# Kernel tuning notes

Hardware: AMD Instinct MI355X
Metric: run time of the kernel (lower is better)

The kernel has to match this reference:

```python
import jax, jax.numpy as jnp
import numpy as np

B, L, DIN, DOUT, H, N, NLAYERS, NRES, NSPECIES = 32, 2048, 5, 5, 256, 32, 4, 3, 100


def conv1d(x, w, b, pad):
    # x: (B, Cin, L), w: (Cout, Cin, K)
    y = jax.lax.conv_general_dilated(x, w, (1,), [(pad, pad)], dimension_numbers=('NCH', 'OIH', 'NCH'))
    return y + b[None, :, None]


def layer_norm_c(x, g, b):
    # LayerNorm over channel dim of (B, H, L) (matches norm(x.transpose(-1,-2)).transpose(-1,-2))
    mu = x.mean(1, keepdims=True)
    v = ((x - mu) ** 2).mean(1, keepdims=True)
    return (x - mu) / jnp.sqrt(v + 1e-5) * g[None, :, None] + b[None, :, None]


def dss_layer(x, log_dt, lam_re, lam_im, W_re, W_im, D, glu_w, glu_b):
    # Bidirectional diagonal state-space (DSS) layer, transposed layout (B, H, L).
    Bb, Hh, Ll = x.shape
    dt = jnp.exp(log_dt)                                  # (H,)
    lam = lam_re + 1j * lam_im                            # (N,) with Re(lam) < 0
    pos = jnp.arange(Ll)
    # Vandermonde: E[h,n,l] = exp(dt[h] * lam[n] * l)
    E = jnp.exp(dt[:, None, None] * lam[None, :, None] * pos[None, None, :])  # (H,N,L) complex
    W = W_re + 1j * W_im                                  # (2,H,N) fwd/bwd kernels
    k = jnp.einsum('chn,hnl->chl', W, E).real             # (2,H,L)
    zpad = jnp.zeros_like(k[0])
    k2 = jnp.concatenate([k[0], zpad], -1) + jnp.concatenate([zpad, k[1][:, ::-1]], -1)  # (H,2L)
    # FFT circular conv of length 2L -> linear conv, keep first L
    y = jnp.fft.irfft(jnp.fft.rfft(x, 2 * Ll) * jnp.fft.rfft(k2, 2 * Ll)[None], 2 * Ll)[..., :Ll]
    y = y + D[None, :, None] * x
    y = jax.nn.gelu(y, approximate=False)
    # postact GLU via position-wise linear H -> 2H
    z = jnp.einsum('oh,bhl->bol', glu_w, y) + glu_b[None, :, None]
    return z[:, :Hh] * jax.nn.sigmoid(z[:, Hh:])


def setup_inputs():
    key = jax.random.key(0)
    ks = jax.random.split(key, 20)
    g = lambda i, shape, s=0.05: jax.random.normal(ks[i], shape, jnp.float32) * s
    inp = {}
    inp['x'] = jax.random.normal(ks[0], (B, DIN, L), jnp.float32)
    inp['xs'] = jax.random.randint(ks[1], (B,), 0, NSPECIES)
    inp['enc_w'] = g(2, (H, DIN, 15))
    inp['enc_b'] = jnp.zeros((H,), jnp.float32)
    inp['res_w1'] = g(3, (NRES, H, H, 3), 0.02)
    inp['res_b1'] = jnp.zeros((NRES, H), jnp.float32)
    inp['res_w2'] = g(4, (NRES, H, H, 3), 0.02)
    inp['res_b2'] = jnp.zeros((NRES, H), jnp.float32)
    inp['log_dt'] = jax.random.uniform(ks[5], (NLAYERS, H), jnp.float32, float(np.log(1e-3)), float(np.log(1e-1)))
    inp['lam_re'] = -(0.1 + jax.random.uniform(ks[6], (NLAYERS, N), jnp.float32))
    inp['lam_im'] = jnp.broadcast_to(jnp.pi * jnp.arange(N, dtype=jnp.float32), (NLAYERS, N)) + 0.0
    inp['W_re'] = g(7, (NLAYERS, 2, H, N), 0.1)
    inp['W_im'] = g(8, (NLAYERS, 2, H, N), 0.1)
    inp['D'] = g(9, (NLAYERS, H), 1.0)
    inp['glu_w'] = g(10, (NLAYERS, 2 * H, H))
    inp['glu_b'] = jnp.zeros((NLAYERS, 2 * H), jnp.float32)
    inp['ln_g'] = jnp.ones((NLAYERS, H), jnp.float32)
    inp['ln_b'] = jnp.zeros((NLAYERS, H), jnp.float32)
    inp['dec_w'] = g(11, (DOUT, H, 15))
    inp['dec_b'] = jnp.zeros((DOUT,), jnp.float32)
    inp['sp_emb'] = g(12, (NSPECIES, H), 0.02)
    inp['h1_w'] = g(13, (128, 256)); inp['h1_b'] = jnp.zeros((128,), jnp.float32)
    inp['h2_w'] = g(14, (64, 128)); inp['h2_b'] = jnp.zeros((64,), jnp.float32)
    inp['h3_w'] = g(15, (32, 64)); inp['h3_b'] = jnp.zeros((32,), jnp.float32)
    inp['h4_w'] = g(16, (1, 32)); inp['h4_b'] = jnp.zeros((1,), jnp.float32)
    return inp


def _forward(x, xs, enc_w, enc_b, res_w1, res_b1, res_w2, res_b2, log_dt, lam_re, lam_im, W_re, W_im, D, glu_w, glu_b, ln_g, ln_b, dec_w, dec_b, sp_emb, h1_w, h1_b, h2_w, h2_b, h3_w, h3_b, h4_w, h4_b):
    h = conv1d(x, enc_w, enc_b, 7)
    for i in range(NRES):  # L1Block resnet stack (dropout/BN are identity at eval)
        r = jax.nn.relu(conv1d(h, res_w1[i], res_b1[i], 1))
        r = conv1d(r, res_w2[i], res_b2[i], 1)
        h = jax.nn.relu(r + h)
    for i in range(NLAYERS):  # post-norm DSS blocks
        z = dss_layer(h, log_dt[i], lam_re[i], lam_im[i], W_re[i], W_im[i], D[i], glu_w[i], glu_b[i])
        h = layer_norm_c(z + h, ln_g[i], ln_b[i])
    h = h + sp_emb[xs][:, :, None]  # species encoder (embed_before=False)
    seq_emb = h
    agg = h.mean(-1)  # (B, H)
    r = jax.nn.elu(agg @ h1_w.T + h1_b)
    r = jax.nn.elu(r @ h2_w.T + h2_b)
    r = jax.nn.elu(r @ h3_w.T + h3_b)
    reg_y = r @ h4_w.T + h4_b
    dec = conv1d(h, dec_w, dec_b, 7)
    return dec, seq_emb, reg_y


def reference(x, xs, enc_w, enc_b, res_w1, res_b1, res_w2, res_b2, log_dt, lam_re, lam_im, W_re, W_im, D, glu_w, glu_b, ln_g, ln_b, dec_w, dec_b, sp_emb, h1_w, h1_b, h2_w, h2_b, h3_w, h3_b, h4_w, h4_b):
    return _forward(x, xs, enc_w, enc_b, res_w1, res_b1, res_w2, res_b2, log_dt, lam_re, lam_im, W_re, W_im, D, glu_w, glu_b, ln_g, ln_b, dec_w, dec_b, sp_emb, h1_w, h1_b, h2_w, h2_b, h3_w, h3_b, h4_w, h4_b)
```

## Files before the change

kernel.cpp:

```cpp
#include <hip/hip_runtime.h>
#include <math.h>

#define B 32
#define L 2048
#define DIN 5
#define DOUT 5
#define H 256
#define NST 32
#define NLAYERS 4
#define NRES 3
#define CHUNK 128
#define NCH 16
#define LSEQ (B*H*L)

typedef __attribute__((ext_vector_type(8))) _Float16 half8;
typedef __attribute__((ext_vector_type(4))) float f32x4;

__device__ __forceinline__ float gelu_exact(float v) {
    return 0.5f * v * (1.0f + erff(v * 0.7071067811865475f));
}
#define SWZ(r) ((((r) ^ ((r) >> 2)) & 3))
#define LDIDX(l, c) ((l)*281 + ((c)>>5)*35 + ((c)&31))

__global__ void k_wenc(const float* __restrict__ ew, _Float16* __restrict__ wenc) {
    int idx = blockIdx.x*256 + threadIdx.x;
    if (idx >= 256*96) return;
    int o = idx / 96, kk = idx % 96;
    int ci = kk >> 4, k = kk & 15;
    float v = (ci < DIN && k < 15) ? ew[(o*DIN + ci)*15 + k] : 0.f;
    wenc[idx] = (_Float16)v;
}

__global__ __launch_bounds__(256) void k_enc(const float* __restrict__ x,
        const _Float16* __restrict__ wenc, const float* __restrict__ bias,
        _Float16* __restrict__ out) {
    __shared__ _Float16 a_lds[3*128*32];
    __shared__ _Float16 b_lds[3*128*32];
    const int tid = threadIdx.x;
    const int mbase = blockIdx.x * 128;
    const int oh = blockIdx.y;
    const int b = mbase >> 11;
    const int lbase = mbase & 2047;
    const int lane = tid & 63;
    const int w = tid >> 6;
    const int wm = (w >> 1) * 64, wn = (w & 1) * 64;
    const int fr = lane & 15, kg = lane >> 4;

    #pragma unroll
    for (int i = 0; i < 6; ++i) {
        int g = i*256 + tid;
        int r = g / 12, rem = g % 12;
        int ks = rem >> 2, q = rem & 3;
        int kk0 = ks*32 + q*8;
        int ci = kk0 >> 4, k0 = kk0 & 15;
        half8 va;
        #pragma unroll
        for (int e = 0; e < 8; ++e) {
            int k = k0 + e;
            int l = lbase + r - 7 + k;
            float v = (ci < DIN && k < 15 && l >= 0 && l < L)
                        ? x[((size_t)(b*DIN + ci))*L + l] : 0.f;
            va[e] = (_Float16)v;
        }
        *(half8*)&a_lds[ks*4096 + r*32 + ((q ^ SWZ(r))*8)] = va;
        uint4 vb = *(const uint4*)&wenc[(size_t)(oh*128 + r)*96 + kk0];
        *(uint4*)&b_lds[ks*4096 + r*32 + ((q ^ SWZ(r))*8)] = vb;
    }
    __syncthreads();
    f32x4 acc[4][4];
    #pragma unroll
    for (int i = 0; i < 4; ++i)
        #pragma unroll
        for (int j = 0; j < 4; ++j)
            #pragma unroll
            for (int k = 0; k < 4; ++k) acc[i][j][k] = 0.f;
    #pragma unroll
    for (int ks = 0; ks < 3; ++ks) {
        half8 af[4], bfr[4];
        #pragma unroll
        for (int mf = 0; mf < 4; ++mf) {
            int ra = wm + mf*16 + fr;
            af[mf] = *(const half8*)&a_lds[ks*4096 + ra*32 + ((kg ^ SWZ(ra))*8)];
        }
        #pragma unroll
        for (int nf = 0; nf < 4; ++nf) {
            int rb = wn + nf*16 + fr;
            bfr[nf] = *(const half8*)&b_lds[ks*4096 + rb*32 + ((kg ^ SWZ(rb))*8)];
        }
        #pragma unroll
        for (int mf = 0; mf < 4; ++mf)
            #pragma unroll
            for (int nf = 0; nf < 4; ++nf)
                acc[mf][nf] = __builtin_amdgcn_mfma_f32_16x16x32_f16(af[mf], bfr[nf], acc[mf][nf], 0, 0, 0);
    }
    #pragma unroll
    for (int nf = 0; nf < 4; ++nf) {
        int o = oh*128 + wn + nf*16 + fr;
        float bo = bias[o];
        #pragma unroll
        for (int mf = 0; mf < 4; ++mf)
            #pragma unroll
            for (int rg = 0; rg < 4; ++rg) {
                size_t m = (size_t)mbase + wm + mf*16 + kg*4 + rg;
                out[m*256 + o] = (_Float16)(acc[mf][nf][rg] + bo);
            }
    }
}

__global__ void k_wpack(const float* __restrict__ w1, const float* __restrict__ w2,
                        _Float16* __restrict__ wpk) {
    int idx = blockIdx.x*256 + threadIdx.x;
    if (idx >= NRES*2*3*65536) return;
    int ci = idx & 255;
    int o  = (idx >> 8) & 255;
    int k  = (idx >> 16) % 3;
    int cv = idx / (3*65536);
    const float* src = (cv & 1) ? w2 : w1;
    wpk[idx] = (_Float16)src[(((cv>>1)*H + o)*H + ci)*3 + k];
}

__global__ __launch_bounds__(256) void k_t_cf16(const _Float16* __restrict__ in,
        _Float16* __restrict__ out) {
    __shared__ float t[64][65];
    int tid = threadIdx.x;
    int l0 = blockIdx.x*64, c0 = blockIdx.y*64, b = blockIdx.z;
    #pragma unroll
    for (int i = 0; i < 16; ++i) {
        int idx = i*256 + tid;
        int l = idx >> 6, c = idx & 63;
        t[c][l] = (float)in[((size_t)b*L + l0 + l)*256 + c0 + c];
    }
    __syncthreads();
    #pragma unroll
    for (int i = 0; i < 16; ++i) {
        int idx = i*256 + tid;
        int c = idx >> 6, l = idx & 63;
        out[((size_t)(b*H + c0 + c))*L + l0 + l] = (_Float16)t[c][l];
    }
}

__global__ __launch_bounds__(256) void k_t16(const _Float16* __restrict__ in,
                                             _Float16* __restrict__ out) {
    __shared__ float t[64][65];
    int tid = threadIdx.x;
    int l0 = blockIdx.x*64, c0 = blockIdx.y*64, b = blockIdx.z;
    #pragma unroll
    for (int i = 0; i < 16; ++i) {
        int idx = i*256 + tid;
        int c = idx >> 6, l = idx & 63;
        t[c][l] = (float)in[((size_t)(b*H + c0 + c))*L + l0 + l];
    }
    __syncthreads();
    #pragma unroll
    for (int i = 0; i < 16; ++i) {
        int idx = i*256 + tid;
        int l = idx >> 6, c = idx & 63;
        out[((size_t)b*L + l0 + l)*256 + c0 + c] = (_Float16)t[c][l];
    }
}

template<bool RESID>
__global__ __launch_bounds__(256, 2) void k_cv3(const _Float16* __restrict__ xin,
        const _Float16* __restrict__ wpk, const float* __restrict__ bias,
        const _Float16* __restrict__ resid, _Float16* __restrict__ out) {
    __shared__ _Float16 a_lds[128*32];
    __shared__ _Float16 b_lds[256*32];
    __shared__ float    ep[32*256];
    const int tid = threadIdx.x;
    const int mbase = blockIdx.x * 128;
    const int lane = tid & 63;
    const int w = tid >> 6;
    const int wm = (w >> 1) * 64, wo = (w & 1) * 128;
    const int fr = lane & 15, kg = lane >> 4;

    const int r0s = tid >> 2, q0 = tid & 3;
    const int sq = SWZ(r0s);
    const int awA0 = r0s*32 + ((q0 ^ sq) * 8);
    const int awA1 = (64 + r0s)*32 + ((q0 ^ SWZ(64 + r0s)) * 8);

    f32x4 acc[4][8];
    #pragma unroll
    for (int i = 0; i < 4; ++i)
        #pragma unroll
        for (int j = 0; j < 8; ++j)
            #pragma unroll
            for (int k = 0; k < 4; ++k) acc[i][j][k] = 0.f;

    uint4 pa0, pa1, pb[4];
    auto loadstep = [&](int kk, uint4& a0, uint4& a1, uint4 (&bb)[4]) {
        const int koff = kk >> 3, cic = kk & 7;
        const int cb = cic*32 + q0*8;
        {
            int m = mbase + r0s;
            int ll = (m & (L-1)) + koff - 1;
            a0 = (ll >= 0 && ll < L) ? *(const uint4*)&xin[((size_t)(m + koff - 1))*256 + cb]
                                     : make_uint4(0,0,0,0);
            int m1 = mbase + 64 + r0s;
            int l1 = (m1 & (L-1)) + koff - 1;
            a1 = (l1 >= 0 && l1 < L) ? *(const uint4*)&xin[((size_t)(m1 + koff - 1))*256 + cb]
                                     : make_uint4(0,0,0,0);
        }
        #pragma unroll
        for (int u = 0; u < 4; ++u)
            bb[u] = *(const uint4*)&wpk[((size_t)(koff*256 + u*64 + r0s))*256 + cb];
    };
    loadstep(0, pa0, pa1, pb);
    for (int kk = 0; kk < 24; ++kk) {
        __syncthreads();
        *(uint4*)&a_lds[awA0] = pa0;
        *(uint4*)&a_lds[awA1] = pa1;
        #pragma unroll
        for (int u = 0; u < 4; ++u)
            *(uint4*)&b_lds[(u*64 + r0s)*32 + ((q0 ^ sq)*8)] = pb[u];
        uint4 na0 = make_uint4(0,0,0,0), na1 = na0, nb[4] = {na0, na0, na0, na0};
        if (kk < 23) loadstep(kk+1, na0, na1, nb);
        __syncthreads();
        half8 af[4];
        #pragma unroll
        for (int mf = 0; mf < 4; ++mf) {
            int ra = wm + mf*16 + fr;
            af[mf] = *(const half8*)&a_lds[ra*32 + ((kg ^ SWZ(ra)) * 8)];
        }
        #pragma unroll
        for (int nf = 0; nf < 8; ++nf) {
            int rb = wo + nf*16 + fr;
            half8 bfr = *(const half8*)&b_lds[rb*32 + ((kg ^ SWZ(rb)) * 8)];
            #pragma unroll
            for (int mf = 0; mf < 4; ++mf)
                acc[mf][nf] = __builtin_amdgcn_mfma_f32_16x16x32_f16(af[mf], bfr, acc[mf][nf], 0, 0, 0);
        }
        pa0 = na0; pa1 = na1;
        #pragma unroll
        for (int u = 0; u < 4; ++u) pb[u] = nb[u];
    }
    float bo8[8];
    #pragma unroll
    for (int nf = 0; nf < 8; ++nf) bo8[nf] = bias[wo + nf*16 + fr];
    const int er = tid >> 3, eoc = (tid & 7) * 32;
    #pragma unroll
    for (int mf = 0; mf < 4; ++mf) {
        __syncthreads();
        #pragma unroll
        for (int nf = 0; nf < 8; ++nf) {
            int o = wo + nf*16 + fr;
            int srb = (w >> 1)*16 + kg*4;
            #pragma unroll
            for (int rg = 0; rg < 4; ++rg)
                ep[(srb + rg)*256 + o] = acc[mf][nf][rg] + bo8[nf];
        }
        __syncthreads();
        size_t m = (size_t)mbase + mf*16 + (er < 16 ? er : 48 + er);
        #pragma unroll
        for (int u = 0; u < 4; ++u) {
            float4 v0 = *(float4*)&ep[er*256 + eoc + u*8];
            float4 v1 = *(float4*)&ep[er*256 + eoc + u*8 + 4];
            float vv[8] = {v0.x, v0.y, v0.z, v0.w, v1.x, v1.y, v1.z, v1.w};
            if (RESID) {
                half8 rv = *(const half8*)&resid[m*256 + eoc + u*8];
                #pragma unroll
                for (int e = 0; e < 8; ++e) vv[e] += (float)rv[e];
            }
            half8 hv;
            #pragma unroll
            for (int e = 0; e < 8; ++e) hv[e] = (_Float16)fmaxf(vv[e], 0.f);
            *(half8*)&out[m*256 + eoc + u*8] = hv;
        }
    }
}

__global__ __launch_bounds__(128) void k_wzp(const float* __restrict__ log_dt,
        const float* __restrict__ lam_re, const float* __restrict__ lam_im,
        _Float16* __restrict__ zp, float4* __restrict__ zwbuf, int layer) {
    int hh = blockIdx.x;
    int t = threadIdx.x;
    int dn = t >> 1, c = t & 1, dir = dn >> 5, n = dn & 31;
    float dt = expf(log_dt[layer*H + hh]);
    float a  = dt * lam_re[layer*NST + n];
    float bi = dt * lam_im[layer*NST + n];
    float er = expf(a);
    float zre = er * cosf(bi), zim = er * sinf(bi);
    if (c == 0 && dir == 0) {
        float eC = expf(a * (float)CHUNK);
        float s, co; sincosf(bi * (float)CHUNK, &s, &co);
        zwbuf[hh*NST + n] = make_float4(zre, zim, eC*co, eC*s);
    }
    _Float16* dst = &zp[(size_t)hh*16384 + t*128];
    float cr = 1.f, ci = 0.f;
    for (int p = 0; p < 128; ++p) {
        float val = c ? ci : cr;
        dst[dir ? p : (127 - p)] = (_Float16)val;
        float nr = cr*zre - ci*zim;
        float ni = cr*zim + ci*zre;
        cr = nr; ci = ni;
    }
}

__global__ __launch_bounds__(128) void k_wkern(const float* __restrict__ log_dt,
        const float* __restrict__ lam_re, const float* __restrict__ lam_im,
        const float* __restrict__ W_re, const float* __restrict__ W_im,
        const float* __restrict__ Dv, const float* __restrict__ gw,
        _Float16* __restrict__ wbig, _Float16* __restrict__ wg, int layer) {
    __shared__ float kf[128], kb[128];
    __shared__ float E[128*129];
    const int hh = blockIdx.x;
    const int t = threadIdx.x;
    float dt = expf(log_dt[layer*H + hh]);
    float skf = 0.f, skb = 0.f;
    for (int n = 0; n < 32; ++n) {
        float a  = dt * lam_re[layer*NST + n];
        float bi = dt * lam_im[layer*NST + n];
        float wfr = W_re[((layer*2+0)*H + hh)*NST + n];
        float wfi = W_im[((layer*2+0)*H + hh)*NST + n];
        float wbr = W_re[((layer*2+1)*H + hh)*NST + n];
        float wbi = W_im[((layer*2+1)*H + hh)*NST + n];
        float e0 = expf(a*t), s0, c0; sincosf(bi*t, &s0, &c0);
        float zr0 = e0*c0, zi0 = e0*s0;
        skf = fmaf(wfr, zr0, skf) - wfi*zi0;
        skb = fmaf(wbr, zr0, skb) - wbi*zi0;
        float e1 = expf(a*(t+1)), s1, c1; sincosf(bi*(t+1), &s1, &c1);
        float zr1 = e1*c1, zi1 = e1*s1;
        E[t*129 + n]      = wfr*zr1 - wfi*zi1;
        E[t*129 + 32 + n] = -(wfr*zi1 + wfi*zr1);
        float e2 = expf(a*(127-t)), s2, c2; sincosf(bi*(127-t), &s2, &c2);
        float zr2 = e2*c2, zi2 = e2*s2;
        E[t*129 + 64 + n] = wbr*zr2 - wbi*zi2;
        E[t*129 + 96 + n] = -(wbr*zi2 + wbi*zr2);
    }
    kf[t] = skf + ((t == 0) ? Dv[layer*H + hh] : 0.f);
    kb[t] = skb;
    __syncthreads();
    _Float16* dst = &wbig[(size_t)hh*32768];
    for (int idx = t; idx < 128*256; idx += 128) {
        int tt = idx >> 8, k = idx & 255;
        float v;
        if (k < 128) v = (k <= tt) ? kf[tt - k] : kb[k - tt - 1];
        else         v = E[tt*129 + (k - 128)];
        dst[idx] = (_Float16)v;
    }
    const float* gsrc = &gw[(size_t)layer*131072 + (size_t)hh*512];
    _Float16* gdst = &wg[(size_t)hh*512];
    for (int j = t; j < 512; j += 128) gdst[j] = (_Float16)gsrc[j];
}

__global__ void k_wdec(const float* __restrict__ dw, _Float16* __restrict__ wdk) {
    int idx = blockIdx.x*256 + threadIdx.x;
    if (idx >= 15*16*256) return;
    int cfull = idx & 255;
    int o = (idx >> 8) & 15;
    int k = idx >> 12;
    float v = (o < DOUT) ? dw[(o*H + cfull)*15 + k] : 0.f;
    int cc = cfull >> 5, cl = cfull & 31;
    int cq = cl >> 3, cb = cl & 7;
    wdk[cc*7680 + (k*16 + o)*32 + ((cq ^ SWZ(o))*8) + cb] = (_Float16)v;
}

__global__ __launch_bounds__(256) void k_dss(const _Float16* __restrict__ hm16,
        const _Float16* __restrict__ zp, const _Float16* __restrict__ wbig,
        const float4* __restrict__ zwb, _Float16* __restrict__ y16, int layer) {
    __shared__ _Float16 xbuf[4*64*32];
    __shared__ _Float16 bbuf[2*128*32];
    __shared__ float    sbuf[64*128];
    _Float16* sb16 = (_Float16*)sbuf;

    const int tid = threadIdx.x;
    const int hh = blockIdx.x;
    const int b0 = blockIdx.y * 4;
    const int lane = tid & 63;
    const int w = tid >> 6;
    const int wn = w * 32;
    const int fr = lane & 15, kg = lane >> 4;

    #pragma unroll
    for (int i = 0; i < 4; ++i) {
        int g = i*256 + tid;
        int m = g >> 4, gi = g & 15;
        int kc = gi >> 2, q = gi & 3;
        uint4 v = *(const uint4*)&hm16[((size_t)((b0 + (m>>4))*H + hh))*L
                                       + (m&15)*128 + kc*32 + q*8];
        *(uint4*)&xbuf[kc*2048 + m*32 + ((q ^ SWZ(m))*8)] = v;
    }

    f32x4 acc1[4][2];
    #pragma unroll
    for (int i = 0; i < 4; ++i)
        #pragma unroll
        for (int j = 0; j < 2; ++j)
            #pragma unroll
            for (int k = 0; k < 4; ++k) acc1[i][j][k] = 0.f;
    const _Float16* zb = &zp[(size_t)hh*16384];
    const int gr0 = tid >> 2, gq0 = tid & 3;
    const int gr1 = 64 + gr0;
    uint4 pb0 = *(const uint4*)&zb[gr0*128 + gq0*8];
    uint4 pb1 = *(const uint4*)&zb[gr1*128 + gq0*8];
    for (int kc = 0; kc < 4; ++kc) {
        __syncthreads();
        *(uint4*)&bbuf[(kc&1)*4096 + gr0*32 + ((gq0 ^ SWZ(gr0))*8)] = pb0;
        *(uint4*)&bbuf[(kc&1)*4096 + gr1*32 + ((gq0 ^ SWZ(gr1))*8)] = pb1;
        if (kc < 3) {
            pb0 = *(const uint4*)&zb[gr0*128 + (kc+1)*32 + gq0*8];
            pb1 = *(const uint4*)&zb[gr1*128 + (kc+1)*32 + gq0*8];
        }
        __syncthreads();
        half8 af[4], bf2[2];
        #pragma unroll
        for (int mf = 0; mf < 4; ++mf) {
            int ra = mf*16 + fr;
            af[mf] = *(const half8*)&xbuf[kc*2048 + ra*32 + ((kg ^ SWZ(ra))*8)];
        }
        #pragma unroll
        for (int nf = 0; nf < 2; ++nf) {
            int rb = wn + nf*16 + fr;
            bf2[nf] = *(const half8*)&bbuf[(kc&1)*4096 + rb*32 + ((kg ^ SWZ(rb))*8)];
        }
        #pragma unroll
        for (int mf = 0; mf < 4; ++mf)
            #pragma unroll
            for (int nf = 0; nf < 2; ++nf)
                acc1[mf][nf] = __builtin_amdgcn_mfma_f32_16x16x32_f16(af[mf], bf2[nf], acc1[mf][nf], 0, 0, 0);
    }
    #pragma unroll
    for (int mf = 0; mf < 4; ++mf)
        #pragma unroll
        for (int nf = 0; nf < 2; ++nf)
            #pragma unroll
            for (int rg = 0; rg < 4; ++rg)
                sbuf[(mf*16 + kg*4 + rg)*128 + wn + nf*16 + fr] = acc1[mf][nf][rg];
    __syncthreads();

    {
        int b_loc = tid >> 6, dn = tid & 63;
        int dir = dn >> 5, n = dn & 31;
        float4 z4 = zwb[hh*NST + n];
        float zcre = z4.z, zcim = z4.w;
        int q1 = n >> 3, e1 = n & 7;
        float pre = 0.f, pim = 0.f;
        for (int s = 0; s < NCH; ++s) {
            int ch = dir ? (NCH - 1 - s) : s;
            int m = b_loc*16 + ch;
            bbuf[(dir*2 + 0)*2048 + m*32 + ((q1 ^ SWZ(m))*8) + e1] = (_Float16)pre;
            bbuf[(dir*2 + 1)*2048 + m*32 + ((q1 ^ SWZ(m))*8) + e1] = (_Float16)pim;
            float cre = sbuf[m*128 + dn*2];
            float cim = sbuf[m*128 + dn*2 + 1];
            float nre = fmaf(zcre, pre, fmaf(-zcim, pim, cre));
            float nim = fmaf(zcre, pim, fmaf(zcim, pre, cim));
            pre = nre; pim = nim;
        }
    }
    __syncthreads();

    f32x4 acc3[4][2];
    #pragma unroll
    for (int i = 0; i < 4; ++i)
        #pragma unroll
        for (int j = 0; j < 2; ++j)
            #pragma unroll
            for (int k = 0; k < 4; ++k) acc3[i][j][k] = 0.f;
    const _Float16* wb = &wbig[(size_t)hh*32768];
    pb0 = *(const uint4*)&wb[gr0*256 + gq0*8];
    pb1 = *(const uint4*)&wb[gr1*256 + gq0*8];
    for (int kc = 0; kc < 8; ++kc) {
        __syncthreads();
        *(uint4*)&sb16[(kc&1)*4096 + gr0*32 + ((gq0 ^ SWZ(gr0))*8)] = pb0;
        *(uint4*)&sb16[(kc&1)*4096 + gr1*32 + ((gq0 ^ SWZ(gr1))*8)] = pb1;
        if (kc < 7) {
            pb0 = *(const uint4*)&wb[gr0*256 + (kc+1)*32 + gq0*8];
            pb1 = *(const uint4*)&wb[gr1*256 + (kc+1)*32 + gq0*8];
        }
        __syncthreads();
        half8 af[4], bf2[2];
        #pragma unroll
        for (int mf = 0; mf < 4; ++mf) {
            int ra = mf*16 + fr;
            af[mf] = (kc < 4)
                ? *(const half8*)&xbuf[kc*2048 + ra*32 + ((kg ^ SWZ(ra))*8)]
                : *(const half8*)&bbuf[(kc-4)*2048 + ra*32 + ((kg ^ SWZ(ra))*8)];
        }
        #pragma unroll
        for (int nf = 0; nf < 2; ++nf) {
            int rb = wn + nf*16 + fr;
            bf2[nf] = *(const half8*)&sb16[(kc&1)*4096 + rb*32 + ((kg ^ SWZ(rb))*8)];
        }
        #pragma unroll
        for (int mf = 0; mf < 4; ++mf)
            #pragma unroll
            for (int nf = 0; nf < 2; ++nf)
                acc3[mf][nf] = __builtin_amdgcn_mfma_f32_16x16x32_f16(af[mf], bf2[nf], acc3[mf][nf], 0, 0, 0);
    }
    __syncthreads();
    _Float16* yst = sb16;
    #pragma unroll
    for (int mf = 0; mf < 4; ++mf) {
        #pragma unroll
        for (int rg = 0; rg < 4; ++rg) {
            int m = mf*16 + kg*4 + rg;
            #pragma unroll
            for (int nf = 0; nf < 2; ++nf) {
                int t = wn + nf*16 + fr;
                yst[m*136 + t] = (_Float16)gelu_exact(acc3[mf][nf][rg]);
            }
        }
    }
    __syncthreads();
    {
        int r = tid >> 2, tc = (tid & 3) * 32;
        size_t gb = ((size_t)((b0 + (r>>4))*H + hh))*L + (r&15)*128;
        #pragma unroll
        for (int u = 0; u < 4; ++u)
            *(half8*)&y16[gb + tc + u*8] = *(half8*)&yst[r*136 + tc + u*8];
    }
}

__global__ __launch_bounds__(256) void k_glu16(const _Float16* __restrict__ yt,
        const _Float16* __restrict__ wg, const float* __restrict__ bias,
        _Float16* __restrict__ zc) {
    __shared__ _Float16 a_lds[128*32];
    __shared__ _Float16 b_lds[128*32];
    __shared__ float    ep[32*64];
    const int tid = threadIdx.x;
    const int mbase = blockIdx.x * 128;
    const int o0 = blockIdx.y * 64;
    const int lane = tid & 63;
    const int w = tid >> 6;
    const int wm = (w >> 1) * 64, wn = (w & 1) * 32;
    const int fr = lane & 15, kg = lane >> 4;
    const int r0s = tid >> 2, q0 = tid & 3;
    const int r1s = 64 + r0s;
    const int aw0 = r0s*32 + ((q0 ^ SWZ(r0s)) * 8);
    const int aw1 = r1s*32 + ((q0 ^ SWZ(r1s)) * 8);
    const int og0 = o0 + r0s;
    const int og1 = 256 + o0 + r0s;

    f32x4 accg[4][2], accs[4][2];
    #pragma unroll
    for (int i = 0; i < 4; ++i)
        #pragma unroll
        for (int j = 0; j < 2; ++j)
            #pragma unroll
            for (int k = 0; k < 4; ++k) { accg[i][j][k] = 0.f; accs[i][j][k] = 0.f; }

    uint4 pa0, pa1, pb0, pb1;
    auto loadstep = [&](int kc, uint4& a0, uint4& a1, uint4& b0, uint4& b1) {
        const int cb = kc*32 + q0*8;
        a0 = *(const uint4*)&yt[((size_t)(mbase + r0s))*256 + cb];
        a1 = *(const uint4*)&yt[((size_t)(mbase + r1s))*256 + cb];
        b0 = *(const uint4*)&wg[((size_t)og0)*256 + cb];
        b1 = *(const uint4*)&wg[((size_t)og1)*256 + cb];
    };
    loadstep(0, pa0, pa1, pb0, pb1);
    for (int kc = 0; kc < 8; ++kc) {
        __syncthreads();
        *(uint4*)&a_lds[aw0] = pa0;
        *(uint4*)&a_lds[aw1] = pa1;
        *(uint4*)&b_lds[aw0] = pb0;
        *(uint4*)&b_lds[aw1] = pb1;
        uint4 na0 = make_uint4(0,0,0,0), na1 = na0, nb0 = na0, nb1 = na0;
        if (kc < 7) loadstep(kc+1, na0, na1, nb0, nb1);
        __syncthreads();
        half8 af[4], bg[2], bs[2];
        #pragma unroll
        for (int mf = 0; mf < 4; ++mf) {
            int ra = wm + mf*16 + fr;
            af[mf] = *(const half8*)&a_lds[ra*32 + ((kg ^ SWZ(ra)) * 8)];
        }
        #pragma unroll
        for (int nf = 0; nf < 2; ++nf) {
            int rb = wn + nf*16 + fr;
            bg[nf] = *(const half8*)&b_lds[rb*32 + ((kg ^ SWZ(rb)) * 8)];
            int rb2 = 64 + rb;
            bs[nf] = *(const half8*)&b_lds[rb2*32 + ((kg ^ SWZ(rb2)) * 8)];
        }
        #pragma unroll
        for (int mf = 0; mf < 4; ++mf)
            #pragma unroll
            for (int nf = 0; nf < 2; ++nf) {
                accg[mf][nf] = __builtin_amdgcn_mfma_f32_16x16x32_f16(af[mf], bg[nf], accg[mf][nf], 0, 0, 0);
                accs[mf][nf] = __builtin_amdgcn_mfma_f32_16x16x32_f16(af[mf], bs[nf], accs[mf][nf], 0, 0, 0);
            }
        pa0 = na0; pa1 = na1; pb0 = nb0; pb1 = nb1;
    }
    float b0v[2], b1v[2];
    #pragma unroll
    for (int nf = 0; nf < 2; ++nf) {
        int o = o0 + wn + nf*16 + fr;
        b0v[nf] = bias[o]; b1v[nf] = bias[256 + o];
    }
    const int er = tid >> 3, eoc = (tid & 7) * 8;
    #pragma unroll
    for (int mf = 0; mf < 4; ++mf) {
        __syncthreads();
        #pragma unroll
        for (int nf = 0; nf < 2; ++nf) {
            int ol = wn + nf*16 + fr;
            int srb = (w >> 1)*16 + kg*4;
            #pragma unroll
            for (int rg = 0; rg < 4; ++rg) {
                float g = accg[mf][nf][rg] + b0v[nf];
                float s = accs[mf][nf][rg] + b1v[nf];
                ep[(srb + rg)*64 + ol] = g / (1.f + expf(-s));
            }
        }
        __syncthreads();
        size_t m = (size_t)mbase + mf*16 + (er < 16 ? er : 48 + er);
        float4 v0 = *(float4*)&ep[er*64 + eoc];
        float4 v1 = *(float4*)&ep[er*64 + eoc + 4];
        half8 hv;
        hv[0]=(_Float16)v0.x; hv[1]=(_Float16)v0.y; hv[2]=(_Float16)v0.z; hv[3]=(_Float16)v0.w;
        hv[4]=(_Float16)v1.x; hv[5]=(_Float16)v1.y; hv[6]=(_Float16)v1.z; hv[7]=(_Float16)v1.w;
        *(half8*)&zc[m*256 + o0 + eoc] = hv;
    }
}

template<bool SP>
__global__ __launch_bounds__(256) void k_ln2(const _Float16* __restrict__ zc,
        _Float16* __restrict__ hm, const float* __restrict__ g, const float* __restrict__ bb,
        const int* __restrict__ xs, const float* __restrict__ emb,
        float* __restrict__ outseq) {
    __shared__ float tl[8992];
    int tid = threadIdx.x;
    int b = blockIdx.y;
    int l0 = blockIdx.x * 32;
    for (int j = tid; j < 1024; j += 256) {
        int c = j >> 2, l8 = (j & 3) * 8;
        half8 v = *(const half8*)&hm[((size_t)(b*H + c))*L + l0 + l8];
        #pragma unroll
        for (int e = 0; e < 8; ++e) tl[LDIDX(l8 + e, c)] = (float)v[e];
    }
    __syncthreads();
    int r = tid >> 3, p = tid & 7;
    float v[32];
    float sum = 0.f, ss = 0.f;
    const _Float16* zrow = &zc[((size_t)(b*L + l0 + r))*256 + p*32];
    #pragma unroll
    for (int q = 0; q < 4; ++q) {
        half8 z8 = *(const half8*)&zrow[q*8];
        #pragma unroll
        for (int i = 0; i < 8; ++i) {
            float hv = tl[LDIDX(r, p*32 + q*8 + i)];
            float vv = (float)z8[i] + hv;
            v[q*8+i] = vv;
            sum += vv; ss = fmaf(vv, vv, ss);
        }
    }
    sum += __shfl_xor(sum, 1); ss += __shfl_xor(ss, 1);
    sum += __shfl_xor(sum, 2); ss += __shfl_xor(ss, 2);
    sum += __shfl_xor(sum, 4); ss += __shfl_xor(ss, 4);
    float mu = sum * (1.f/256.f);
    float var = ss * (1.f/256.f) - mu*mu;
    float rs = rsqrtf(var + 1e-5f);
    int sp = SP ? xs[b] : 0;
    #pragma unroll
    for (int q = 0; q < 32; ++q) {
        int c = p*32 + q;
        float val = (v[q] - mu) * rs * g[c] + bb[c];
        if (SP) val += emb[sp*H + c];
        tl[LDIDX(r, c)] = val;
    }
    __syncthreads();
    for (int j = tid; j < 1024; j += 256) {
        int c = j >> 2, l8 = (j & 3) * 8;
        float fv[8];
        half8 hv;
        #pragma unroll
        for (int e = 0; e < 8; ++e) {
            fv[e] = tl[LDIDX(l8 + e, c)];
            hv[e] = (_Float16)fv[e];
        }
        *(half8*)&hm[((size_t)(b*H + c))*L + l0 + l8] = hv;
        if (SP) {
            *(float4*)&outseq[((size_t)(b*H + c))*L + l0 + l8] = make_float4(fv[0],fv[1],fv[2],fv[3]);
            *(float4*)&outseq[((size_t)(b*H + c))*L + l0 + l8 + 4] = make_float4(fv[4],fv[5],fv[6],fv[7]);
        }
    }
}

__global__ __launch_bounds__(128) void k_dec(const _Float16* __restrict__ ht,
        const _Float16* __restrict__ wdk, const float* __restrict__ bias,
        float* __restrict__ outdec) {
    __shared__ _Float16 a_lds[160*32];
    __shared__ _Float16 b_lds[15*16*32];
    const int tid = threadIdx.x;
    const int mbase = blockIdx.x * 128;
    const int b = mbase >> 11;
    const int lbase = mbase & 2047;
    const int lane = tid & 63;
    const int w = tid >> 6;
    const int fr = lane & 15, kg = lane >> 4;
    const int rs = tid >> 2, q0 = tid & 3;
    f32x4 acc[4];
    #pragma unroll
    for (int i = 0; i < 4; ++i)
        #pragma unroll
        for (int k = 0; k < 4; ++k) acc[i][k] = 0.f;
    for (int cc = 0; cc < 8; ++cc) {
        __syncthreads();
        #pragma unroll
        for (int ps = 0; ps < 5; ++ps) {
            int r = ps*32 + rs;
            if (r < 142) {
                int l = lbase - 7 + r;
                uint4 v = (l >= 0 && l < L) ? *(const uint4*)&ht[((size_t)(b*L + l))*256 + cc*32 + q0*8]
                                            : make_uint4(0,0,0,0);
                *(uint4*)&a_lds[r*32 + ((q0 ^ SWZ(r))*8)] = v;
            }
        }
        for (int jj = tid; jj < 960; jj += 128)
            *(uint4*)&b_lds[jj*8] = *(const uint4*)&wdk[cc*7680 + jj*8];
        __syncthreads();
        #pragma unroll
        for (int k = 0; k < 15; ++k) {
            half8 bfr = *(const half8*)&b_lds[(k*16 + fr)*32 + ((kg ^ SWZ(fr))*8)];
            #pragma unroll
            for (int mf = 0; mf < 4; ++mf) {
                int ra = w*64 + mf*16 + fr + k;
                half8 af = *(const half8*)&a_lds[ra*32 + ((kg ^ SWZ(ra))*8)];
                acc[mf] = __builtin_amdgcn_mfma_f32_16x16x32_f16(af, bfr, acc[mf], 0, 0, 0);
            }
        }
    }
    if (fr < DOUT) {
        float bo = bias[fr];
        #pragma unroll
        for (int mf = 0; mf < 4; ++mf)
            #pragma unroll
            for (int rg = 0; rg < 4; ++rg) {
                int m = mbase + w*64 + mf*16 + kg*4 + rg;
                outdec[((size_t)(b*DOUT + fr))*L + (m & 2047)] = acc[mf][rg] + bo;
            }
    }
}

__global__ __launch_bounds__(256) void k_agg(const _Float16* __restrict__ h, float* __restrict__ agg) {
    __shared__ float red[256];
    int bc = blockIdx.x;
    int tid = threadIdx.x;
    half8 v = *(const half8*)&h[(size_t)bc*L + tid*8];
    float s = 0.f;
    #pragma unroll
    for (int e = 0; e < 8; ++e) s += (float)v[e];
    red[tid] = s; __syncthreads();
    for (int k = 128; k > 0; k >>= 1) {
        if (tid < k) red[tid] += red[tid+k];
        __syncthreads();
    }
    if (tid == 0) agg[bc] = red[0] * (1.f/(float)L);
}

__global__ __launch_bounds__(128) void k_mlp(const float* __restrict__ agg,
        const float* __restrict__ w1, const float* __restrict__ b1,
        const float* __restrict__ w2, const float* __restrict__ b2,
        const float* __restrict__ w3, const float* __restrict__ b3,
        const float* __restrict__ w4, const float* __restrict__ b4,
        float* __restrict__ outreg) {
    __shared__ float a0[256], r1[128], r2[64], r3[32];
    int b = blockIdx.x, tid = threadIdx.x;
    a0[tid] = agg[b*256 + tid];
    a0[tid+128] = agg[b*256 + tid + 128];
    __syncthreads();
    {
        float s = b1[tid];
        for (int k = 0; k < 256; ++k) s = fmaf(w1[tid*256+k], a0[k], s);
        r1[tid] = s > 0.f ? s : expm1f(s);
    }
    __syncthreads();
    if (tid < 64) {
        float s = b2[tid];
        for (int k = 0; k < 128; ++k) s = fmaf(w2[tid*128+k], r1[k], s);
        r2[tid] = s > 0.f ? s : expm1f(s);
    }
    __syncthreads();
    if (tid < 32) {
        float s = b3[tid];
        for (int k = 0; k < 64; ++k) s = fmaf(w3[tid*64+k], r2[k], s);
        r3[tid] = s > 0.f ? s : expm1f(s);
    }
    __syncthreads();
    if (tid == 0) {
        float s = b4[0];
        for (int k = 0; k < 32; ++k) s = fmaf(w4[k], r3[k], s);
        outreg[b] = s;
    }
}

extern "C" void kernel_launch(void* const* d_in, const int* in_sizes, int n_in,
                              void* d_out, int out_size, void* d_ws, size_t ws_size,
                              hipStream_t stream) {
    const float* x      = (const float*)d_in[0];
    const int*   xs     = (const int*)d_in[1];
    const float* enc_w  = (const float*)d_in[2];
    const float* enc_b  = (const float*)d_in[3];
    const float* res_w1 = (const float*)d_in[4];
    const float* res_b1 = (const float*)d_in[5];
    const float* res_w2 = (const float*)d_in[6];
    const float* res_b2 = (const float*)d_in[7];
    const float* log_dt = (const float*)d_in[8];
    const float* lam_re = (const float*)d_in[9];
    const float* lam_im = (const float*)d_in[10];
    const float* W_re   = (const float*)d_in[11];
    const float* W_im   = (const float*)d_in[12];
    const float* Dv     = (const float*)d_in[13];
    const float* glu_w  = (const float*)d_in[14];
    const float* glu_b  = (const float*)d_in[15];
    const float* ln_g   = (const float*)d_in[16];
    const float* ln_b   = (const float*)d_in[17];
    const float* dec_w  = (const float*)d_in[18];
    const float* dec_b  = (const float*)d_in[19];
    const float* sp_emb = (const float*)d_in[20];
    const float* h1_w = (const float*)d_in[21]; const float* h1_b = (const float*)d_in[22];
    const float* h2_w = (const float*)d_in[23]; const float* h2_b = (const float*)d_in[24];
    const float* h3_w = (const float*)d_in[25]; const float* h3_b = (const float*)d_in[26];
    const float* h4_w = (const float*)d_in[27]; const float* h4_b = (const float*)d_in[28];

    float* ws   = (float*)d_ws;
    _Float16* hm16 = (_Float16*)ws;
    float* t1   = ws + (size_t)LSEQ;
    float* t2   = ws + (size_t)2*LSEQ;
    _Float16* xb  = (_Float16*)t1;
    _Float16* xa  = (_Float16*)t1 + (size_t)LSEQ;
    _Float16* wpk = (_Float16*)t2;
    _Float16* yt   = (_Float16*)t1;
    _Float16* wbig = (_Float16*)t1 + (size_t)LSEQ;
    _Float16* zp   = wbig + (size_t)H*32768;
    _Float16* y16  = (_Float16*)t2;
    _Float16* zc16 = (_Float16*)t2;
    _Float16* dect = (_Float16*)t1;
    float* tail = ws + (size_t)3*LSEQ;
    _Float16* wg  = (_Float16*)tail;
    float4* zwb = (float4*)(tail + 65536);
    float* aggb = tail + 65536 + 32768;
    _Float16* wdk = (_Float16*)(aggb + 8192);
    _Float16* wenc = wdk + 61440;

    float* outdec = (float*)d_out;
    float* outseq = outdec + B*DOUT*L;
    float* outreg = outseq + (size_t)LSEQ;

    k_wenc<<<96, 256, 0, stream>>>(enc_w, wenc);
    k_enc<<<dim3(B*L/128, 2), 256, 0, stream>>>(x, wenc, enc_b, xa);

    k_wpack<<<(NRES*2*3*65536 + 255)/256, 256, 0, stream>>>(res_w1, res_w2, wpk);
    for (int r = 0; r < NRES; ++r) {
        k_cv3<false><<<B*L/128, 256, 0, stream>>>(
            xa, wpk + (size_t)(r*2+0)*3*65536, res_b1 + r*H, nullptr, xb);
        k_cv3<true><<<B*L/128, 256, 0, stream>>>(
            xb, wpk + (size_t)(r*2+1)*3*65536, res_b2 + r*H, xa, xa);
    }
    k_t_cf16<<<dim3(L/64, H/64, B), 256, 0, stream>>>(xa, hm16);

    for (int i = 0; i < NLAYERS; ++i) {
        k_wzp<<<H, 128, 0, stream>>>(log_dt, lam_re, lam_im, zp, zwb, i);
        k_wkern<<<H, 128, 0, stream>>>(log_dt, lam_re, lam_im, W_re, W_im, Dv, glu_w,
                                       wbig, wg, i);
        k_dss<<<dim3(H, 8), 256, 0, stream>>>(hm16, zp, wbig, zwb, y16, i);
        k_t16<<<dim3(L/64, H/64, B), 256, 0, stream>>>(y16, yt);
        k_glu16<<<dim3(B*L/128, 4), 256, 0, stream>>>(yt, wg, glu_b + i*512, zc16);
        if (i < NLAYERS - 1)
            k_ln2<false><<<dim3(L/32, B), 256, 0, stream>>>(zc16, hm16, ln_g + i*H, ln_b + i*H,
                                                            nullptr, nullptr, nullptr);
        else
            k_ln2<true><<<dim3(L/32, B), 256, 0, stream>>>(zc16, hm16, ln_g + i*H, ln_b + i*H,
                                                           xs, sp_emb, outseq);
    }

    k_agg<<<B*H, 256, 0, stream>>>(hm16, aggb);
    k_mlp<<<B, 128, 0, stream>>>(aggb, h1_w, h1_b, h2_w, h2_b, h3_w, h3_b, h4_w, h4_b, outreg);
    k_t16<<<dim3(L/64, H/64, B), 256, 0, stream>>>(hm16, dect);
    k_wdec<<<(15*16*256 + 255)/256, 256, 0, stream>>>(dec_w, wdk);
    k_dec<<<B*L/128, 128, 0, stream>>>(dect, wdk, dec_b, outdec);
}
```

Before: 1.126 ms.

## Halve batch tile in DSS kernel and restructure double-buffered pipeline with one barrier

The DSS chunked-scan kernel now processes 2 batches per block instead of 4, which doubles the grid and shrinks LDS and accumulator use so more blocks fit per CU (launch_bounds 256,4). The double-buffered weight staging loops are restructured to prefetch one stage ahead with a single barrier per iteration instead of two. Half the threads now sit idle during the serial scan phase. Weight tiles are reloaded twice as often in aggregate.

```diff
diff --git a/kernel.cpp b/kernel.cpp
--- a/kernel.cpp
+++ b/kernel.cpp
@@ -354,35 +354,35 @@
     wdk[cc*7680 + (k*16 + o)*32 + ((cq ^ SWZ(o))*8) + cb] = (_Float16)v;
 }
 
-__global__ __launch_bounds__(256) void k_dss(const _Float16* __restrict__ hm16,
+__global__ __launch_bounds__(256, 4) void k_dss(const _Float16* __restrict__ hm16,
         const _Float16* __restrict__ zp, const _Float16* __restrict__ wbig,
         const float4* __restrict__ zwb, _Float16* __restrict__ y16, int layer) {
-    __shared__ _Float16 xbuf[4*64*32];
+    __shared__ _Float16 xbuf[4*32*32];
     __shared__ _Float16 bbuf[2*128*32];
-    __shared__ float    sbuf[64*128];
+    __shared__ float    sbuf[32*128];
     _Float16* sb16 = (_Float16*)sbuf;
 
     const int tid = threadIdx.x;
     const int hh = blockIdx.x;
-    const int b0 = blockIdx.y * 4;
+    const int b0 = blockIdx.y * 2;
     const int lane = tid & 63;
     const int w = tid >> 6;
     const int wn = w * 32;
     const int fr = lane & 15, kg = lane >> 4;
 
     #pragma unroll
-    for (int i = 0; i < 4; ++i) {
+    for (int i = 0; i < 2; ++i) {
         int g = i*256 + tid;
         int m = g >> 4, gi = g & 15;
         int kc = gi >> 2, q = gi & 3;
         uint4 v = *(const uint4*)&hm16[((size_t)((b0 + (m>>4))*H + hh))*L
                                        + (m&15)*128 + kc*32 + q*8];
-        *(uint4*)&xbuf[kc*2048 + m*32 + ((q ^ SWZ(m))*8)] = v;
-    }
-
-    f32x4 acc1[4][2];
-    #pragma unroll
-    for (int i = 0; i < 4; ++i)
+        *(uint4*)&xbuf[kc*1024 + m*32 + ((q ^ SWZ(m))*8)] = v;
+    }
+
+    f32x4 acc1[2][2];
+    #pragma unroll
+    for (int i = 0; i < 2; ++i)
         #pragma unroll
         for (int j = 0; j < 2; ++j)
             #pragma unroll
@@ -390,22 +390,29 @@
     const _Float16* zb = &zp[(size_t)hh*16384];
     const int gr0 = tid >> 2, gq0 = tid & 3;
     const int gr1 = 64 + gr0;
+    const int bw0 = gr0*32 + ((gq0 ^ SWZ(gr0))*8);
+    const int bw1 = gr1*32 + ((gq0 ^ SWZ(gr1))*8);
     uint4 pb0 = *(const uint4*)&zb[gr0*128 + gq0*8];
     uint4 pb1 = *(const uint4*)&zb[gr1*128 + gq0*8];
+    *(uint4*)&bbuf[bw0] = pb0;
+    *(uint4*)&bbuf[bw1] = pb1;
+    pb0 = *(const uint4*)&zb[gr0*128 + 32 + gq0*8];
+    pb1 = *(const uint4*)&zb[gr1*128 + 32 + gq0*8];
+    __syncthreads();
     for (int kc = 0; kc < 4; ++kc) {
-        __syncthreads();
-        *(uint4*)&bbuf[(kc&1)*4096 + gr0*32 + ((gq0 ^ SWZ(gr0))*8)] = pb0;
-        *(uint4*)&bbuf[(kc&1)*4096 + gr1*32 + ((gq0 ^ SWZ(gr1))*8)] = pb1;
         if (kc < 3) {
-            pb0 = *(const uint4*)&zb[gr0*128 + (kc+1)*32 + gq0*8];
-            pb1 = *(const uint4*)&zb[gr1*128 + (kc+1)*32 + gq0*8];
-        }
-        __syncthreads();
-        half8 af[4], bf2[2];
-        #pragma unroll
-        for (int mf = 0; mf < 4; ++mf) {
+            *(uint4*)&bbuf[((kc+1)&1)*4096 + bw0] = pb0;
+            *(uint4*)&bbuf[((kc+1)&1)*4096 + bw1] = pb1;
+            if (kc < 2) {
+                pb0 = *(const uint4*)&zb[gr0*128 + (kc+2)*32 + gq0*8];
+                pb1 = *(const uint4*)&zb[gr1*128 + (kc+2)*32 + gq0*8];
+            }
+        }
+        half8 af[2], bf2[2];
+        #pragma unroll
+        for (int mf = 0; mf < 2; ++mf) {
             int ra = mf*16 + fr;
-            af[mf] = *(const half8*)&xbuf[kc*2048 + ra*32 + ((kg ^ SWZ(ra))*8)];
+            af[mf] = *(const half8*)&xbuf[kc*1024 + ra*32 + ((kg ^ SWZ(ra))*8)];
         }
         #pragma unroll
         for (int nf = 0; nf < 2; ++nf) {
@@ -413,13 +420,14 @@
             bf2[nf] = *(const half8*)&bbuf[(kc&1)*4096 + rb*32 + ((kg ^ SWZ(rb))*8)];
         }
         #pragma unroll
-        for (int mf = 0; mf < 4; ++mf)
+        for (int mf = 0; mf < 2; ++mf)
             #pragma unroll
             for (int nf = 0; nf < 2; ++nf)
                 acc1[mf][nf] = __builtin_amdgcn_mfma_f32_16x16x32_f16(af[mf], bf2[nf], acc1[mf][nf], 0, 0, 0);
-    }
-    #pragma unroll
-    for (int mf = 0; mf < 4; ++mf)
+        __syncthreads();
+    }
+    #pragma unroll
+    for (int mf = 0; mf < 2; ++mf)
         #pragma unroll
         for (int nf = 0; nf < 2; ++nf)
             #pragma unroll
@@ -429,28 +437,30 @@
 
     {
         int b_loc = tid >> 6, dn = tid & 63;
-        int dir = dn >> 5, n = dn & 31;
-        float4 z4 = zwb[hh*NST + n];
-        float zcre = z4.z, zcim = z4.w;
-        int q1 = n >> 3, e1 = n & 7;
-        float pre = 0.f, pim = 0.f;
-        for (int s = 0; s < NCH; ++s) {
-            int ch = dir ? (NCH - 1 - s) : s;
-            int m = b_loc*16 + ch;
-            bbuf[(dir*2 + 0)*2048 + m*32 + ((q1 ^ SWZ(m))*8) + e1] = (_Float16)pre;
-            bbuf[(dir*2 + 1)*2048 + m*32 + ((q1 ^ SWZ(m))*8) + e1] = (_Float16)pim;
-            float cre = sbuf[m*128 + dn*2];
-            float cim = sbuf[m*128 + dn*2 + 1];
-            float nre = fmaf(zcre, pre, fmaf(-zcim, pim, cre));
-            float nim = fmaf(zcre, pim, fmaf(zcim, pre, cim));
-            pre = nre; pim = nim;
-        }
-    }
-    __syncthreads();
-
-    f32x4 acc3[4][2];
-    #pragma unroll
-    for (int i = 0; i < 4; ++i)
+        if (b_loc < 2) {
+            int dir = dn >> 5, n = dn & 31;
+            float4 z4 = zwb[hh*NST + n];
+            float zcre = z4.z, zcim = z4.w;
+            int q1 = n >> 3, e1 = n & 7;
+            float pre = 0.f, pim = 0.f;
+            for (int s = 0; s < NCH; ++s) {
+                int ch = dir ? (NCH - 1 - s) : s;
+                int m = b_loc*16 + ch;
+                bbuf[(dir*2 + 0)*1024 + m*32 + ((q1 ^ SWZ(m))*8) + e1] = (_Float16)pre;
+                bbuf[(dir*2 + 1)*1024 + m*32 + ((q1 ^ SWZ(m))*8) + e1] = (_Float16)pim;
+                float cre = sbuf[m*128 + dn*2];
+                float cim = sbuf[m*128 + dn*2 + 1];
+                float nre = fmaf(zcre, pre, fmaf(-zcim, pim, cre));
+                float nim = fmaf(zcre, pim, fmaf(zcim, pre, cim));
+                pre = nre; pim = nim;
+            }
+        }
+    }
+    __syncthreads();
+
+    f32x4 acc3[2][2];
+    #pragma unroll
+    for (int i = 0; i < 2; ++i)
         #pragma unroll
         for (int j = 0; j < 2; ++j)
             #pragma unroll
@@ -458,22 +468,27 @@
     const _Float16* wb = &wbig[(size_t)hh*32768];
     pb0 = *(const uint4*)&wb[gr0*256 + gq0*8];
     pb1 = *(const uint4*)&wb[gr1*256 + gq0*8];
+    *(uint4*)&sb16[bw0] = pb0;
+    *(uint4*)&sb16[bw1] = pb1;
+    pb0 = *(const uint4*)&wb[gr0*256 + 32 + gq0*8];
+    pb1 = *(const uint4*)&wb[gr1*256 + 32 + gq0*8];
+    __syncthreads();
     for (int kc = 0; kc < 8; ++kc) {
-        __syncthreads();
-        *(uint4*)&sb16[(kc&1)*4096 + gr0*32 + ((gq0 ^ SWZ(gr0))*8)] = pb0;
-        *(uint4*)&sb16[(kc&1)*4096 + gr1*32 + ((gq0 ^ SWZ(gr1))*8)] = pb1;
         if (kc < 7) {
-            pb0 = *(const uint4*)&wb[gr0*256 + (kc+1)*32 + gq0*8];
-            pb1 = *(const uint4*)&wb[gr1*256 + (kc+1)*32 + gq0*8];
-        }
-        __syncthreads();
-        half8 af[4], bf2[2];
-        #pragma unroll
-        for (int mf = 0; mf < 4; ++mf) {
+            *(uint4*)&sb16[((kc+1)&1)*4096 + bw0] = pb0;
+            *(uint4*)&sb16[((kc+1)&1)*4096 + bw1] = pb1;
+            if (kc < 6) {
+                pb0 = *(const uint4*)&wb[gr0*256 + (kc+2)*32 + gq0*8];
+                pb1 = *(const uint4*)&wb[gr1*256 + (kc+2)*32 + gq0*8];
+            }
+        }
+        half8 af[2], bf2[2];
+        #pragma unroll
+        for (int mf = 0; mf < 2; ++mf) {
             int ra = mf*16 + fr;
             af[mf] = (kc < 4)
-                ? *(const half8*)&xbuf[kc*2048 + ra*32 + ((kg ^ SWZ(ra))*8)]
-                : *(const half8*)&bbuf[(kc-4)*2048 + ra*32 + ((kg ^ SWZ(ra))*8)];
+                ? *(const half8*)&xbuf[kc*1024 + ra*32 + ((kg ^ SWZ(ra))*8)]
+                : *(const half8*)&bbuf[(kc-4)*1024 + ra*32 + ((kg ^ SWZ(ra))*8)];
         }
         #pragma unroll
         for (int nf = 0; nf < 2; ++nf) {
@@ -481,15 +496,15 @@
             bf2[nf] = *(const half8*)&sb16[(kc&1)*4096 + rb*32 + ((kg ^ SWZ(rb))*8)];
         }
         #pragma unroll
-        for (int mf = 0; mf < 4; ++mf)
+        for (int mf = 0; mf < 2; ++mf)
             #pragma unroll
             for (int nf = 0; nf < 2; ++nf)
                 acc3[mf][nf] = __builtin_amdgcn_mfma_f32_16x16x32_f16(af[mf], bf2[nf], acc3[mf][nf], 0, 0, 0);
-    }
-    __syncthreads();
+        __syncthreads();
+    }
     _Float16* yst = sb16;
     #pragma unroll
-    for (int mf = 0; mf < 4; ++mf) {
+    for (int mf = 0; mf < 2; ++mf) {
         #pragma unroll
         for (int rg = 0; rg < 4; ++rg) {
             int m = mf*16 + kg*4 + rg;
@@ -502,11 +517,10 @@
     }
     __syncthreads();
     {
-        int r = tid >> 2, tc = (tid & 3) * 32;
+        int r = tid >> 3, tc = (tid & 7) * 16;
         size_t gb = ((size_t)((b0 + (r>>4))*H + hh))*L + (r&15)*128;
-        #pragma unroll
-        for (int u = 0; u < 4; ++u)
-            *(half8*)&y16[gb + tc + u*8] = *(half8*)&yst[r*136 + tc + u*8];
+        *(half8*)&y16[gb + tc]     = *(half8*)&yst[r*136 + tc];
+        *(half8*)&y16[gb + tc + 8] = *(half8*)&yst[r*136 + tc + 8];
     }
 }
 
@@ -850,7 +864,7 @@
         k_wzp<<<H, 128, 0, stream>>>(log_dt, lam_re, lam_im, zp, zwb, i);
         k_wkern<<<H, 128, 0, stream>>>(log_dt, lam_re, lam_im, W_re, W_im, Dv, glu_w,
                                        wbig, wg, i);
-        k_dss<<<dim3(H, 8), 256, 0, stream>>>(hm16, zp, wbig, zwb, y16, i);
+        k_dss<<<dim3(H, 16), 256, 0, stream>>>(hm16, zp, wbig, zwb, y16, i);
         k_t16<<<dim3(L/64, H/64, B), 256, 0, stream>>>(y16, yt);
         k_glu16<<<dim3(B*L/128, 4), 256, 0, stream>>>(yt, wg, glu_b + i*512, zc16);
         if (i < NLAYERS - 1)
```

New measurement: 1.092 ms. -3.0%, faster.
